# Optimization experiments

Measured on AMD Instinct MI355X. Metric: run time of the kernel, lower is better.

Reference implementation:

```python
import jax, jax.numpy as jnp
import numpy as np

DIM = 768
HEADS = 12
HEAD_DIM = DIM // HEADS
HIDDEN = 4 * DIM
SCALE = HEAD_DIM ** -0.5
LN_EPS = 1e-5


def layer_norm(x, g, b):
    mu = jnp.mean(x, axis=-1, keepdims=True)
    var = jnp.var(x, axis=-1, keepdims=True)
    return (x - mu) * jax.lax.rsqrt(var + LN_EPS) * g + b


def setup_inputs() -> dict:
    key = jax.random.key(0)
    ks = jax.random.split(key, 10)
    B, N = 2, 2048
    s = 0.02
    return {
        "x": jax.random.normal(ks[0], (B, N, DIM), jnp.float32),
        "elevation": jax.random.uniform(ks[1], (B, N), jnp.float32),
        "qkv_w": jax.random.normal(ks[2], (DIM, 3 * DIM), jnp.float32) * s,
        "qkv_b": jnp.zeros((3 * DIM,), jnp.float32),
        "proj_w": jax.random.normal(ks[3], (DIM, DIM), jnp.float32) * s,
        "proj_b": jnp.zeros((DIM,), jnp.float32),
        "ln1_g": jnp.ones((DIM,), jnp.float32),
        "ln1_b": jnp.zeros((DIM,), jnp.float32),
        "ln2_g": jnp.ones((DIM,), jnp.float32),
        "ln2_b": jnp.zeros((DIM,), jnp.float32),
        "fc1_w": jax.random.normal(ks[4], (DIM, HIDDEN), jnp.float32) * s,
        "fc1_b": jnp.zeros((HIDDEN,), jnp.float32),
        "fc2_w": jax.random.normal(ks[5], (HIDDEN, DIM), jnp.float32) * s,
        "fc2_b": jnp.zeros((DIM,), jnp.float32),
        "barrier": jnp.asarray(3.0, jnp.float32),
    }


def reference(x, elevation, qkv_w, qkv_b, proj_w, proj_b, ln1_g, ln1_b,
              ln2_g, ln2_b, fc1_w, fc1_b, fc2_w, fc2_b, barrier):
    B, N, C = x.shape
    h = layer_norm(x, ln1_g, ln1_b)
    qkv = (h @ qkv_w + qkv_b).reshape(B, N, 3, HEADS, HEAD_DIM)
    q, k, v = jnp.moveaxis(qkv, 2, 0)  # each [B, N, H, D]
    # scores: [B, H, N, N]
    scores = jnp.einsum('bnhd,bmhd->bhnm', q, k) * SCALE
    w = jax.nn.softmax(scores, axis=-1)
    # pairwise elevation mask [B, N, N]: sigmoid(-s * (elev_j - elev_i))
    diff = elevation[:, None, :] - elevation[:, :, None]
    mask = jnp.clip(jax.nn.sigmoid(-barrier * diff), 1e-6, 1.0)
    w = w * mask[:, None, :, :]
    w = w / (jnp.sum(w, axis=-1, keepdims=True) + 1e-8)
    attn_out = jnp.einsum('bhnm,bmhd->bnhd', w, v).reshape(B, N, C)
    x = x + attn_out @ proj_w + proj_b
    h2 = layer_norm(x, ln2_g, ln2_b)
    mlp = jax.nn.gelu(h2 @ fc1_w + fc1_b, approximate=False) @ fc2_w + fc2_b
    return x + mlp
```

## Files before the change

kernel.cpp:

```cpp
#include <hip/hip_runtime.h>
#include <math.h>

#define DIM 768
#define HEADS 12
#define SEQ 2048
#define ROWS 4096
#define LN_EPS 1e-5f

typedef __attribute__((ext_vector_type(8))) short short8;
typedef __attribute__((ext_vector_type(4))) float floatx4;
typedef __attribute__((ext_vector_type(16))) float floatx16;
typedef unsigned short ushort_t;

__device__ __forceinline__ ushort_t f2bf(float x) {
    unsigned u = __float_as_uint(x);
    u += 0x7fff + ((u >> 16) & 1);
    return (ushort_t)(u >> 16);
}

__device__ __forceinline__ void gload_lds16(const void* g, void* l) {
    __builtin_amdgcn_global_load_lds((const __attribute__((address_space(1))) void*)g,
                                     (__attribute__((address_space(3))) void*)l, 16, 0, 0);
}

__launch_bounds__(256)
__global__ void prep_all(const float* __restrict__ w0, const float* __restrict__ w1,
                         const float* __restrict__ w2, const float* __restrict__ w3,
                         ushort_t* __restrict__ t0, ushort_t* __restrict__ t1,
                         ushort_t* __restrict__ t2, ushort_t* __restrict__ t3,
                         const float* __restrict__ elev, const float* __restrict__ barrier_p,
                         float* __restrict__ G, float* __restrict__ C2,
                         const float* __restrict__ x, const float* __restrict__ ln1_g,
                         const float* __restrict__ ln1_b, ushort_t* __restrict__ h) {
    __shared__ __align__(16) ushort_t s[64][72];
    int bid = blockIdx.x;
    int t = threadIdx.x;
    if (bid < 1728) {
        const float* W; ushort_t* WT; int K, N, nx, id;
        if (bid < 432)       { W = w0; WT = t0; K = 768;  N = 2304; nx = 36; id = bid; }
        else if (bid < 576)  { W = w1; WT = t1; K = 768;  N = 768;  nx = 12; id = bid - 432; }
        else if (bid < 1152) { W = w2; WT = t2; K = 768;  N = 3072; nx = 48; id = bid - 576; }
        else                 { W = w3; WT = t3; K = 3072; N = 768;  nx = 12; id = bid - 1152; }
        int tx = id % nx, ty = id / nx;
        int k0 = ty * 64, n0 = tx * 64;
        int rr0 = t >> 4, c4 = (t & 15) * 4;
        for (int rr = rr0; rr < 64; rr += 16) {
            float4 w = *(const float4*)(W + (size_t)(k0 + rr) * N + n0 + c4);
            s[c4 + 0][rr] = f2bf(w.x); s[c4 + 1][rr] = f2bf(w.y);
            s[c4 + 2][rr] = f2bf(w.z); s[c4 + 3][rr] = f2bf(w.w);
        }
        __syncthreads();
        int nl = t >> 2, kq = (t & 3) * 16;
        uint4 a = *(const uint4*)&s[nl][kq];
        uint4 b = *(const uint4*)&s[nl][kq + 8];
        *(uint4*)(WT + (size_t)(n0 + nl) * K + k0 + kq) = a;
        *(uint4*)(WT + (size_t)(n0 + nl) * K + k0 + kq + 8) = b;
    } else if (bid < 1744) {
        int i = (bid - 1728) * 256 + t;
        float be = barrier_p[0] * elev[i];
        G[i]  = __expf(be);
        C2[i] = be;
    } else {
        int row = bid - 1744;
        const float* xr = x + (size_t)row * DIM;
        float v0 = xr[t], v1 = xr[t + 256], v2 = xr[t + 512];
        float sm  = v0 + v1 + v2;
        float ss = v0 * v0 + v1 * v1 + v2 * v2;
        #pragma unroll
        for (int o = 32; o >= 1; o >>= 1) { sm += __shfl_xor(sm, o); ss += __shfl_xor(ss, o); }
        __shared__ float rs[4], rss[4];
        int wid = t >> 6, lane = t & 63;
        if (lane == 0) { rs[wid] = sm; rss[wid] = ss; }
        __syncthreads();
        if (t == 0) {
            float S = 0.f, SS = 0.f;
            for (int i2 = 0; i2 < 4; i2++) { S += rs[i2]; SS += rss[i2]; }
            rs[0] = S; rss[0] = SS;
        }
        __syncthreads();
        float mean = rs[0] * (1.0f / DIM);
        float var  = rss[0] * (1.0f / DIM) - mean * mean;
        float rstd = rsqrtf(var + LN_EPS);
        ushort_t* orow = h + (size_t)row * DIM;
        orow[t]       = f2bf((v0 - mean) * rstd * ln1_g[t]       + ln1_b[t]);
        orow[t + 256] = f2bf((v1 - mean) * rstd * ln1_g[t + 256] + ln1_b[t + 256]);
        orow[t + 512] = f2bf((v2 - mean) * rstd * ln1_g[t + 512] + ln1_b[t + 512]);
    }
}

__launch_bounds__(256)
__global__ void ln_kernel(const float* __restrict__ x, const float* __restrict__ g,
                          const float* __restrict__ b, ushort_t* __restrict__ out) {
    int row = blockIdx.x;
    const float* xr = x + (size_t)row * DIM;
    int t = threadIdx.x;
    float v0 = xr[t], v1 = xr[t + 256], v2 = xr[t + 512];
    float s  = v0 + v1 + v2;
    float ss = v0 * v0 + v1 * v1 + v2 * v2;
    #pragma unroll
    for (int o = 32; o >= 1; o >>= 1) { s += __shfl_xor(s, o); ss += __shfl_xor(ss, o); }
    __shared__ float rs[4], rss[4];
    int wid = t >> 6, lane = t & 63;
    if (lane == 0) { rs[wid] = s; rss[wid] = ss; }
    __syncthreads();
    if (t == 0) {
        float S = 0.f, SS = 0.f;
        for (int i = 0; i < 4; i++) { S += rs[i]; SS += rss[i]; }
        rs[0] = S; rss[0] = SS;
    }
    __syncthreads();
    float mean = rs[0] * (1.0f / DIM);
    float var  = rss[0] * (1.0f / DIM) - mean * mean;
    float rstd = rsqrtf(var + LN_EPS);
    ushort_t* orow = out + (size_t)row * DIM;
    orow[t]       = f2bf((v0 - mean) * rstd * g[t]       + b[t]);
    orow[t + 256] = f2bf((v1 - mean) * rstd * g[t + 256] + b[t + 256]);
    orow[t + 512] = f2bf((v2 - mean) * rstd * g[t + 512] + b[t + 512]);
}


#define G16_PREFETCH(K0, SA, SB)                                                      \
    {                                                                                 \
        int c0_ = t, r0_ = c0_ >> 2, bl0_ = c0_ & 3;                                  \
        int sw0_ = bl0_ ^ ((r0_ ^ (r0_ >> 2)) & 3);                                   \
        gload_lds16(A  + (size_t)(row0 + r0_) * K + (K0) + (sw0_ << 3), &SA[c0_ * 8]); \
        gload_lds16(WT + (size_t)(col0 + r0_) * K + (K0) + (sw0_ << 3), &SB[c0_ * 8]); \
        int c1_ = 256 + t, r1_ = c1_ >> 2, bl1_ = c1_ & 3;                            \
        int sw1_ = bl1_ ^ ((r1_ ^ (r1_ >> 2)) & 3);                                   \
        gload_lds16(A  + (size_t)(row0 + r1_) * K + (K0) + (sw1_ << 3), &SA[c1_ * 8]); \
        gload_lds16(WT + (size_t)(col0 + r1_) * K + (K0) + (sw1_ << 3), &SB[c1_ * 8]); \
    }

#define G16_COMPUTE(SA, SB)                                                           \
    {                                                                                 \
        short8 a_[4], b_[4];                                                          \
        _Pragma("unroll")                                                             \
        for (int i = 0; i < 4; i++) {                                                 \
            int ra_ = wm * 64 + i * 16 + cl;                                          \
            a_[i] = *(const short8*)&SA[ra_ * 32 + ((quad ^ ((ra_ ^ (ra_ >> 2)) & 3)) << 3)]; \
        }                                                                             \
        _Pragma("unroll")                                                             \
        for (int j = 0; j < 4; j++) {                                                 \
            int rb_ = wn * 64 + j * 16 + cl;                                          \
            b_[j] = *(const short8*)&SB[rb_ * 32 + ((quad ^ ((rb_ ^ (rb_ >> 2)) & 3)) << 3)]; \
        }                                                                             \
        _Pragma("unroll")                                                             \
        for (int i = 0; i < 4; i++)                                                   \
            _Pragma("unroll")                                                         \
            for (int j = 0; j < 4; j++)                                               \
                acc[i][j] = __builtin_amdgcn_mfma_f32_16x16x32_bf16(a_[i], b_[j], acc[i][j], 0, 0, 0); \
    }

template<int EPI>
__launch_bounds__(256)
__global__ void gemm16(const ushort_t* __restrict__ A, const ushort_t* __restrict__ WT,
                       const float* __restrict__ bias, ushort_t* __restrict__ outB,
                       ushort_t* __restrict__ qb, ushort_t* __restrict__ kb,
                       ushort_t* __restrict__ vb, int N, int K) {
    __shared__ __align__(16) ushort_t sA0[128 * 32];
    __shared__ __align__(16) ushort_t sA1[128 * 32];
    __shared__ __align__(16) ushort_t sB0[128 * 32];
    __shared__ __align__(16) ushort_t sB1[128 * 32];
    int t = threadIdx.x;
    int row0 = blockIdx.y * 128, col0 = blockIdx.x * 128;
    int wid = t >> 6, lane = t & 63;
    int wm = wid >> 1, wn = wid & 1;
    int cl = lane & 15, quad = lane >> 4;

    floatx4 acc[4][4];
    #pragma unroll
    for (int i = 0; i < 4; i++)
        #pragma unroll
        for (int j = 0; j < 4; j++) { floatx4 z = {0.f, 0.f, 0.f, 0.f}; acc[i][j] = z; }

    G16_PREFETCH(0, sA0, sB0)
    for (int k0 = 0; k0 < K; k0 += 64) {
        __syncthreads();
        if (k0 + 32 < K) G16_PREFETCH(k0 + 32, sA1, sB1)
        G16_COMPUTE(sA0, sB0)
        __syncthreads();
        if (k0 + 64 < K) G16_PREFETCH(k0 + 64, sA0, sB0)
        G16_COMPUTE(sA1, sB1)
    }

    #pragma unroll
    for (int i = 0; i < 4; i++) {
        #pragma unroll
        for (int j = 0; j < 4; j++) {
            int gcol = col0 + wn * 64 + j * 16 + cl;
            float bv = bias[gcol];
            #pragma unroll
            for (int rg = 0; rg < 4; rg++) {
                int grow = row0 + wm * 64 + i * 16 + quad * 4 + rg;
                float v = acc[i][j][rg] + bv;
                if (EPI == 0) {
                    int which = gcol / 768;
                    int hc = gcol - which * 768;
                    int hh = hc >> 6, d = hc & 63;
                    int b_ = grow >> 11, n = grow & 2047;
                    size_t bhh = (size_t)(b_ * 12 + hh);
                    if (which == 0)      qb[(bhh * 2048 + n) * 64 + d] = f2bf(v * 0.125f);
                    else if (which == 1) kb[(bhh * 2048 + n) * 64 + d] = f2bf(v);
                    else                 vb[(bhh * 64 + d) * 2048 + n] = f2bf(v);
                } else {
                    v = 0.5f * v * (1.f + erff(v * 0.70710678118654752f));
                    outB[(size_t)grow * N + gcol] = f2bf(v);
                }
            }
        }
    }
}

#define GB_PREFETCH(K0, SA, SB)                                                       \
    {                                                                                 \
        int r_ = t >> 2, sub_ = t & 3;                                                \
        gload_lds16(A  + (size_t)(row0 + r_) * K + (K0) + sub_ * 8, &SA[t * 8]);      \
        gload_lds16(WT + (size_t)(col0 + r_) * K + (K0) + sub_ * 8, &SB[t * 8]);      \
    }

#define GB_COMPUTE(SA, SB)                                                            \
    {                                                                                 \
        short8 a_[2], b_[2];                                                          \
        _Pragma("unroll")                                                             \
        for (int i = 0; i < 2; i++)                                                   \
            a_[i] = *(const short8*)&SA[(wm * 32 + i * 16 + cl) * 32 + quad * 8];     \
        _Pragma("unroll")                                                             \
        for (int j = 0; j < 2; j++)                                                   \
            b_[j] = *(const short8*)&SB[(wn * 32 + j * 16 + cl) * 32 + quad * 8];     \
        _Pragma("unroll")                                                             \
        for (int i = 0; i < 2; i++)                                                   \
            _Pragma("unroll")                                                         \
            for (int j = 0; j < 2; j++)                                               \
                acc[i][j] = __builtin_amdgcn_mfma_f32_16x16x32_bf16(a_[i], b_[j], acc[i][j], 0, 0, 0); \
    }

__launch_bounds__(256)
__global__ void gemm_bf16(const ushort_t* __restrict__ A, const ushort_t* __restrict__ WT,
                          const float* __restrict__ bias, const float* __restrict__ res,
                          float* __restrict__ outF, int N, int K) {
    __shared__ __align__(16) ushort_t sA0[64 * 32];
    __shared__ __align__(16) ushort_t sA1[64 * 32];
    __shared__ __align__(16) ushort_t sB0[64 * 32];
    __shared__ __align__(16) ushort_t sB1[64 * 32];
    int t = threadIdx.x;
    int row0 = blockIdx.y * 64, col0 = blockIdx.x * 64;
    int wid = t >> 6, lane = t & 63;
    int wm = wid >> 1, wn = wid & 1;
    int cl = lane & 15, quad = lane >> 4;

    floatx4 acc[2][2];
    #pragma unroll
    for (int i = 0; i < 2; i++)
        #pragma unroll
        for (int j = 0; j < 2; j++) { floatx4 z = {0.f, 0.f, 0.f, 0.f}; acc[i][j] = z; }

    GB_PREFETCH(0, sA0, sB0)
    for (int k0 = 0; k0 < K; k0 += 64) {
        __syncthreads();
        if (k0 + 32 < K) GB_PREFETCH(k0 + 32, sA1, sB1)
        GB_COMPUTE(sA0, sB0)
        __syncthreads();
        if (k0 + 64 < K) GB_PREFETCH(k0 + 64, sA0, sB0)
        GB_COMPUTE(sA1, sB1)
    }

    #pragma unroll
    for (int i = 0; i < 2; i++) {
        #pragma unroll
        for (int j = 0; j < 2; j++) {
            int gcol = col0 + wn * 32 + j * 16 + cl;
            float bv = bias[gcol];
            #pragma unroll
            for (int rg = 0; rg < 4; rg++) {
                int grow = row0 + wm * 32 + i * 16 + quad * 4 + rg;
                float v = acc[i][j][rg] + bv + res[(size_t)grow * N + gcol];
                outF[(size_t)grow * N + gcol] = v;
            }
        }
    }
}

#define PREFETCH(K0N, KSN, VTN)                                                   \
    {                                                                             \
        const ushort_t* kbase_ = kb + (bh * 2048 + (K0N)) * 64;                   \
        const ushort_t* vbase_ = vb + bh * 131072 + (K0N);                        \
        int c0_ = t, r0_ = c0_ >> 3, b0_ = c0_ & 7;                               \
        gload_lds16(kbase_ + (r0_ << 6) + ((b0_ ^ (r0_ & 7)) << 3), &KSN[c0_ * 8]); \
        gload_lds16(vbase_ + (size_t)r0_ * 2048 + ((b0_ ^ (r0_ & 7)) << 3), &VTN[c0_ * 8]); \
        int c1_ = 256 + t, r1_ = c1_ >> 3, b1_ = c1_ & 7;                         \
        gload_lds16(kbase_ + (r1_ << 6) + ((b1_ ^ (r1_ & 7)) << 3), &KSN[c1_ * 8]); \
        gload_lds16(vbase_ + (size_t)r1_ * 2048 + ((b1_ ^ (r1_ & 7)) << 3), &VTN[c1_ * 8]); \
    }

#define ATTN_TILE(KT, KSC, VTC, KSN, VTN)                                         \
    {                                                                             \
        __syncthreads();                                                          \
        if ((KT) < 31) PREFETCH(((KT) + 1) * 64, KSN, VTN)                        \
        float gjv_[4];                                                            \
        gjv_[0] = G[b * 2048 + (KT) * 64 + cl];                                   \
        gjv_[1] = G[b * 2048 + (KT) * 64 + 16 + cl];                              \
        gjv_[2] = G[b * 2048 + (KT) * 64 + 32 + cl];                              \
        gjv_[3] = G[b * 2048 + (KT) * 64 + 48 + cl];                              \
        floatx4 s_[4];                                                            \
        s_[0] = c2init; s_[1] = c2init; s_[2] = c2init; s_[3] = c2init;           \
        _Pragma("unroll")                                                         \
        for (int kh = 0; kh < 2; kh++) {                                          \
            short8 aq_ = *(const short8*)&Qs[((wid * 16 + cl) << 6) + (((kh * 4 + quad) ^ (cl & 7)) << 3)]; \
            _Pragma("unroll")                                                     \
            for (int nt = 0; nt < 4; nt++) {                                      \
                short8 bk_ = *(const short8*)&KSC[((nt * 16 + cl) << 6) + (((kh * 4 + quad) ^ (cl & 7)) << 3)]; \
                s_[nt] = __builtin_amdgcn_mfma_f32_16x16x32_bf16(aq_, bk_, s_[nt], 0, 0, 0); \
            }                                                                     \
        }                                                                         \
        _Pragma("unroll")                                                         \
        for (int rg = 0; rg < 4; rg++) {                                          \
            int prow_ = wid * 16 + quad * 4 + rg;                                 \
            int r8_ = prow_ & 7, pb_ = prow_ << 6, cs_ = cl & 7, ch_ = cl >> 3;   \
            _Pragma("unroll")                                                     \
            for (int nt = 0; nt < 4; nt++) {                                      \
                float tf_ = __expf(s_[nt][rg]);                                   \
                float p_  = tf_ * __builtin_amdgcn_rcpf(gi[rg] + gjv_[nt]);       \
                sem[rg] += p_;                                                    \
                Ps[pb_ + (((nt * 2 + ch_) ^ r8_) << 3) + cs_] = (ushort_t)(__float_as_uint(p_) >> 16); \
            }                                                                     \
        }                                                                         \
        _Pragma("unroll")                                                         \
        for (int kh = 0; kh < 2; kh++) {                                          \
            short8 ap_ = *(const short8*)&Ps[((wid * 16 + cl) << 6) + (((kh * 4 + quad) ^ (cl & 7)) << 3)]; \
            _Pragma("unroll")                                                     \
            for (int dt = 0; dt < 4; dt++) {                                      \
                short8 bv_ = *(const short8*)&VTC[((dt * 16 + cl) << 6) + (((kh * 4 + quad) ^ (cl & 7)) << 3)]; \
                o[dt] = __builtin_amdgcn_mfma_f32_16x16x32_bf16(ap_, bv_, o[dt], 0, 0, 0); \
            }                                                                     \
        }                                                                         \
    }

__launch_bounds__(256)
__global__ void attn_mfma(const ushort_t* __restrict__ qb, const ushort_t* __restrict__ kb,
                          const ushort_t* __restrict__ vb, const float* __restrict__ G,
                          const float* __restrict__ C2, ushort_t* __restrict__ attn) {
    __shared__ __align__(16) ushort_t Qs[4096];
    __shared__ __align__(16) ushort_t Ks0[4096];
    __shared__ __align__(16) ushort_t Ks1[4096];
    __shared__ __align__(16) ushort_t Vt0[4096];
    __shared__ __align__(16) ushort_t Vt1[4096];
    __shared__ __align__(16) ushort_t Ps[4096];
    int qt = blockIdx.x, h = blockIdx.y, b = blockIdx.z;
    int t = threadIdx.x, wid = t >> 6, lane = t & 63;
    int cl = lane & 15, quad = lane >> 4;
    int q0 = qt * 64;
    size_t bh = (size_t)(b * 12 + h);

    const ushort_t* qbase = qb + (bh * 2048 + q0) * 64;
    #pragma unroll
    for (int i = 0; i < 2; i++) {
        int c = i * 256 + t, row = c >> 3, blk = c & 7;
        gload_lds16(qbase + (row << 6) + ((blk ^ (row & 7)) << 3), &Qs[c * 8]);
    }
    int qrow4 = b * 2048 + q0 + wid * 16 + quad * 4;
    float4 g4  = *(const float4*)(G  + qrow4);
    float4 c24 = *(const float4*)(C2 + qrow4);
    float gi[4]  = {g4.x, g4.y, g4.z, g4.w};
    floatx4 c2init = {c24.x, c24.y, c24.z, c24.w};

    PREFETCH(0, Ks0, Vt0)

    floatx4 o[4];
    #pragma unroll
    for (int j = 0; j < 4; j++) { floatx4 z = {0.f, 0.f, 0.f, 0.f}; o[j] = z; }
    float sem[4] = {0.f, 0.f, 0.f, 0.f};

    for (int kt = 0; kt < 32; kt += 2) {
        ATTN_TILE(kt,     Ks0, Vt0, Ks1, Vt1)
        ATTN_TILE(kt + 1, Ks1, Vt1, Ks0, Vt0)
    }

    #pragma unroll
    for (int rg = 0; rg < 4; rg++) {
        float m = sem[rg];
        #pragma unroll
        for (int off = 1; off < 16; off <<= 1) m += __shfl_xor(m, off);
        float inv = __builtin_amdgcn_rcpf(m);
        int grow = b * 2048 + q0 + wid * 16 + quad * 4 + rg;
        #pragma unroll
        for (int dt = 0; dt < 4; dt++)
            attn[(size_t)grow * 768 + h * 64 + dt * 16 + cl] = f2bf(o[dt][rg] * inv);
    }
}

extern "C" void kernel_launch(void* const* d_in, const int* in_sizes, int n_in,
                              void* d_out, int out_size, void* d_ws, size_t ws_size,
                              hipStream_t stream) {
    const float* x      = (const float*)d_in[0];
    const float* elev   = (const float*)d_in[1];
    const float* qkv_w  = (const float*)d_in[2];
    const float* qkv_b  = (const float*)d_in[3];
    const float* proj_w = (const float*)d_in[4];
    const float* proj_b = (const float*)d_in[5];
    const float* ln1_g  = (const float*)d_in[6];
    const float* ln1_b  = (const float*)d_in[7];
    const float* ln2_g  = (const float*)d_in[8];
    const float* ln2_b  = (const float*)d_in[9];
    const float* fc1_w  = (const float*)d_in[10];
    const float* fc1_b  = (const float*)d_in[11];
    const float* fc2_w  = (const float*)d_in[12];
    const float* fc2_b  = (const float*)d_in[13];
    const float* barrier= (const float*)d_in[14];
    float* out = (float*)d_out;
    char* ws = (char*)d_ws;

    ushort_t* h    = (ushort_t*)(ws + 0);
    ushort_t* qb   = (ushort_t*)(ws + 6291456);
    ushort_t* kb   = (ushort_t*)(ws + 12582912);
    ushort_t* vb   = (ushort_t*)(ws + 18874368);
    ushort_t* f1   = (ushort_t*)(ws + 0);
    ushort_t* attn = (ushort_t*)(ws + 25165824);
    ushort_t* h2   = (ushort_t*)(ws + 31457280);
    float*    Gf   = (float*)(ws + 31457280);
    float*    C2f  = (float*)(ws + 31473664);
    ushort_t* qkvT = (ushort_t*)(ws + 37748736);
    ushort_t* projT= (ushort_t*)(ws + 41287680);
    ushort_t* fc1T = (ushort_t*)(ws + 42467328);
    ushort_t* fc2T = (ushort_t*)(ws + 47185920);

    prep_all<<<5840, 256, 0, stream>>>(qkv_w, proj_w, fc1_w, fc2_w, qkvT, projT, fc1T, fc2T,
                                       elev, barrier, Gf, C2f, x, ln1_g, ln1_b, h);
    gemm16<0><<<dim3(2304 / 128, 32), 256, 0, stream>>>(
        h, qkvT, qkv_b, nullptr, qb, kb, vb, 2304, 768);
    attn_mfma<<<dim3(32, HEADS, 2), 256, 0, stream>>>(qb, kb, vb, Gf, C2f, attn);
    gemm_bf16<<<dim3(768 / 64, 64), 256, 0, stream>>>(
        attn, projT, proj_b, x, out, 768, 768);
    ln_kernel<<<ROWS, 256, 0, stream>>>(out, ln2_g, ln2_b, h2);
    gemm16<1><<<dim3(3072 / 128, 32), 256, 0, stream>>>(
        h2, fc1T, fc1_b, f1, nullptr, nullptr, nullptr, 3072, 768);
    gemm_bf16<<<dim3(768 / 64, 64), 256, 0, stream>>>(
        f1, fc2T, fc2_b, out, out, 768, 3072);
}
```

Measured before the change: 312.8 us.

## Load GEMM A fragments from global into registers, hoist attention Q fragments

In both GEMM kernels the A operand no longer goes through LDS. Each wave loads its A fragments straight from global memory into registers, one K-step ahead, while B stays double-buffered in LDS. This halves LDS traffic and LDS footprint, but the two waves that share the same A rows now each fetch them from global/L2, and the accesses are strided 16-byte row reads. In the attention kernel, the Q fragments are read from LDS once into registers before the loop, and the per-tile barrier moves from the start of each tile to its end.

```diff
diff --git a/kernel.cpp b/kernel.cpp
--- a/kernel.cpp
+++ b/kernel.cpp
@@ -9,7 +9,6 @@
 
 typedef __attribute__((ext_vector_type(8))) short short8;
 typedef __attribute__((ext_vector_type(4))) float floatx4;
-typedef __attribute__((ext_vector_type(16))) float floatx16;
 typedef unsigned short ushort_t;
 
 __device__ __forceinline__ ushort_t f2bf(float x) {
@@ -119,36 +118,35 @@
 }
 
 
-#define G16_PREFETCH(K0, SA, SB)                                                      \
+#define G16_PREB(K0, SB)                                                              \
     {                                                                                 \
         int c0_ = t, r0_ = c0_ >> 2, bl0_ = c0_ & 3;                                  \
         int sw0_ = bl0_ ^ ((r0_ ^ (r0_ >> 2)) & 3);                                   \
-        gload_lds16(A  + (size_t)(row0 + r0_) * K + (K0) + (sw0_ << 3), &SA[c0_ * 8]); \
         gload_lds16(WT + (size_t)(col0 + r0_) * K + (K0) + (sw0_ << 3), &SB[c0_ * 8]); \
         int c1_ = 256 + t, r1_ = c1_ >> 2, bl1_ = c1_ & 3;                            \
         int sw1_ = bl1_ ^ ((r1_ ^ (r1_ >> 2)) & 3);                                   \
-        gload_lds16(A  + (size_t)(row0 + r1_) * K + (K0) + (sw1_ << 3), &SA[c1_ * 8]); \
         gload_lds16(WT + (size_t)(col0 + r1_) * K + (K0) + (sw1_ << 3), &SB[c1_ * 8]); \
     }
 
-#define G16_COMPUTE(SA, SB)                                                           \
-    {                                                                                 \
-        short8 a_[4], b_[4];                                                          \
-        _Pragma("unroll")                                                             \
-        for (int i = 0; i < 4; i++) {                                                 \
-            int ra_ = wm * 64 + i * 16 + cl;                                          \
-            a_[i] = *(const short8*)&SA[ra_ * 32 + ((quad ^ ((ra_ ^ (ra_ >> 2)) & 3)) << 3)]; \
+#define G16_LOADA(K0, AR)                                                             \
+    {                                                                                 \
+        _Pragma("unroll")                                                             \
+        for (int i_ = 0; i_ < 4; i_++) AR[i_] = *(const short8*)(Arow[i_] + (K0));    \
+    }
+
+#define G16_COMP(AR, SB)                                                              \
+    {                                                                                 \
+        short8 b_[4];                                                                 \
+        _Pragma("unroll")                                                             \
+        for (int j_ = 0; j_ < 4; j_++) {                                              \
+            int rb_ = wn * 64 + j_ * 16 + cl;                                         \
+            b_[j_] = *(const short8*)&SB[rb_ * 32 + ((quad ^ ((rb_ ^ (rb_ >> 2)) & 3)) << 3)]; \
         }                                                                             \
         _Pragma("unroll")                                                             \
-        for (int j = 0; j < 4; j++) {                                                 \
-            int rb_ = wn * 64 + j * 16 + cl;                                          \
-            b_[j] = *(const short8*)&SB[rb_ * 32 + ((quad ^ ((rb_ ^ (rb_ >> 2)) & 3)) << 3)]; \
-        }                                                                             \
-        _Pragma("unroll")                                                             \
-        for (int i = 0; i < 4; i++)                                                   \
+        for (int i_ = 0; i_ < 4; i_++)                                                \
             _Pragma("unroll")                                                         \
-            for (int j = 0; j < 4; j++)                                               \
-                acc[i][j] = __builtin_amdgcn_mfma_f32_16x16x32_bf16(a_[i], b_[j], acc[i][j], 0, 0, 0); \
+            for (int j_ = 0; j_ < 4; j_++)                                            \
+                acc[i_][j_] = __builtin_amdgcn_mfma_f32_16x16x32_bf16(AR[i_], b_[j_], acc[i_][j_], 0, 0, 0); \
     }
 
 template<int EPI>
@@ -157,8 +155,6 @@
                        const float* __restrict__ bias, ushort_t* __restrict__ outB,
                        ushort_t* __restrict__ qb, ushort_t* __restrict__ kb,
                        ushort_t* __restrict__ vb, int N, int K) {
-    __shared__ __align__(16) ushort_t sA0[128 * 32];
-    __shared__ __align__(16) ushort_t sA1[128 * 32];
     __shared__ __align__(16) ushort_t sB0[128 * 32];
     __shared__ __align__(16) ushort_t sB1[128 * 32];
     int t = threadIdx.x;
@@ -167,20 +163,29 @@
     int wm = wid >> 1, wn = wid & 1;
     int cl = lane & 15, quad = lane >> 4;
 
+    const ushort_t* Arow[4];
+    #pragma unroll
+    for (int i = 0; i < 4; i++)
+        Arow[i] = A + (size_t)(row0 + wm * 64 + i * 16 + cl) * K + quad * 8;
+
     floatx4 acc[4][4];
     #pragma unroll
     for (int i = 0; i < 4; i++)
         #pragma unroll
         for (int j = 0; j < 4; j++) { floatx4 z = {0.f, 0.f, 0.f, 0.f}; acc[i][j] = z; }
 
-    G16_PREFETCH(0, sA0, sB0)
+    short8 aA[4], aB[4];
+    G16_PREB(0, sB0)
+    G16_LOADA(0, aA)
     for (int k0 = 0; k0 < K; k0 += 64) {
         __syncthreads();
-        if (k0 + 32 < K) G16_PREFETCH(k0 + 32, sA1, sB1)
-        G16_COMPUTE(sA0, sB0)
-        __syncthreads();
-        if (k0 + 64 < K) G16_PREFETCH(k0 + 64, sA0, sB0)
-        G16_COMPUTE(sA1, sB1)
+        if (k0 + 32 < K) G16_PREB(k0 + 32, sB1)
+        G16_LOADA(k0 + 32 < K ? k0 + 32 : 0, aB)
+        G16_COMP(aA, sB0)
+        __syncthreads();
+        if (k0 + 64 < K) G16_PREB(k0 + 64, sB0)
+        G16_LOADA(k0 + 64 < K ? k0 + 64 : 0, aA)
+        G16_COMP(aB, sB1)
     }
 
     #pragma unroll
@@ -211,35 +216,35 @@
     }
 }
 
-#define GB_PREFETCH(K0, SA, SB)                                                       \
+#define GB_PREB(K0, SB)                                                               \
     {                                                                                 \
         int r_ = t >> 2, sub_ = t & 3;                                                \
-        gload_lds16(A  + (size_t)(row0 + r_) * K + (K0) + sub_ * 8, &SA[t * 8]);      \
         gload_lds16(WT + (size_t)(col0 + r_) * K + (K0) + sub_ * 8, &SB[t * 8]);      \
     }
 
-#define GB_COMPUTE(SA, SB)                                                            \
-    {                                                                                 \
-        short8 a_[2], b_[2];                                                          \
-        _Pragma("unroll")                                                             \
-        for (int i = 0; i < 2; i++)                                                   \
-            a_[i] = *(const short8*)&SA[(wm * 32 + i * 16 + cl) * 32 + quad * 8];     \
-        _Pragma("unroll")                                                             \
-        for (int j = 0; j < 2; j++)                                                   \
-            b_[j] = *(const short8*)&SB[(wn * 32 + j * 16 + cl) * 32 + quad * 8];     \
-        _Pragma("unroll")                                                             \
-        for (int i = 0; i < 2; i++)                                                   \
+#define GB_LOADA(K0, AR)                                                              \
+    {                                                                                 \
+        _Pragma("unroll")                                                             \
+        for (int i_ = 0; i_ < 2; i_++) AR[i_] = *(const short8*)(Arow[i_] + (K0));    \
+    }
+
+#define GB_COMP(AR, SB)                                                               \
+    {                                                                                 \
+        short8 b_[2];                                                                 \
+        _Pragma("unroll")                                                             \
+        for (int j_ = 0; j_ < 2; j_++)                                                \
+            b_[j_] = *(const short8*)&SB[(wn * 32 + j_ * 16 + cl) * 32 + quad * 8];   \
+        _Pragma("unroll")                                                             \
+        for (int i_ = 0; i_ < 2; i_++)                                                \
             _Pragma("unroll")                                                         \
-            for (int j = 0; j < 2; j++)                                               \
-                acc[i][j] = __builtin_amdgcn_mfma_f32_16x16x32_bf16(a_[i], b_[j], acc[i][j], 0, 0, 0); \
+            for (int j_ = 0; j_ < 2; j_++)                                            \
+                acc[i_][j_] = __builtin_amdgcn_mfma_f32_16x16x32_bf16(AR[i_], b_[j_], acc[i_][j_], 0, 0, 0); \
     }
 
 __launch_bounds__(256)
 __global__ void gemm_bf16(const ushort_t* __restrict__ A, const ushort_t* __restrict__ WT,
                           const float* __restrict__ bias, const float* __restrict__ res,
                           float* __restrict__ outF, int N, int K) {
-    __shared__ __align__(16) ushort_t sA0[64 * 32];
-    __shared__ __align__(16) ushort_t sA1[64 * 32];
     __shared__ __align__(16) ushort_t sB0[64 * 32];
     __shared__ __align__(16) ushort_t sB1[64 * 32];
     int t = threadIdx.x;
@@ -248,20 +253,29 @@
     int wm = wid >> 1, wn = wid & 1;
     int cl = lane & 15, quad = lane >> 4;
 
+    const ushort_t* Arow[2];
+    #pragma unroll
+    for (int i = 0; i < 2; i++)
+        Arow[i] = A + (size_t)(row0 + wm * 32 + i * 16 + cl) * K + quad * 8;
+
     floatx4 acc[2][2];
     #pragma unroll
     for (int i = 0; i < 2; i++)
         #pragma unroll
         for (int j = 0; j < 2; j++) { floatx4 z = {0.f, 0.f, 0.f, 0.f}; acc[i][j] = z; }
 
-    GB_PREFETCH(0, sA0, sB0)
+    short8 aA[2], aB[2];
+    GB_PREB(0, sB0)
+    GB_LOADA(0, aA)
     for (int k0 = 0; k0 < K; k0 += 64) {
         __syncthreads();
-        if (k0 + 32 < K) GB_PREFETCH(k0 + 32, sA1, sB1)
-        GB_COMPUTE(sA0, sB0)
-        __syncthreads();
-        if (k0 + 64 < K) GB_PREFETCH(k0 + 64, sA0, sB0)
-        GB_COMPUTE(sA1, sB1)
+        if (k0 + 32 < K) GB_PREB(k0 + 32, sB1)
+        GB_LOADA(k0 + 32 < K ? k0 + 32 : 0, aB)
+        GB_COMP(aA, sB0)
+        __syncthreads();
+        if (k0 + 64 < K) GB_PREB(k0 + 64, sB0)
+        GB_LOADA(k0 + 64 < K ? k0 + 64 : 0, aA)
+        GB_COMP(aB, sB1)
     }
 
     #pragma unroll
@@ -294,7 +308,6 @@
 
 #define ATTN_TILE(KT, KSC, VTC, KSN, VTN)                                         \
     {                                                                             \
-        __syncthreads();                                                          \
         if ((KT) < 31) PREFETCH(((KT) + 1) * 64, KSN, VTN)                        \
         float gjv_[4];                                                            \
         gjv_[0] = G[b * 2048 + (KT) * 64 + cl];                                   \
@@ -305,7 +318,7 @@
         s_[0] = c2init; s_[1] = c2init; s_[2] = c2init; s_[3] = c2init;           \
         _Pragma("unroll")                                                         \
         for (int kh = 0; kh < 2; kh++) {                                          \
-            short8 aq_ = *(const short8*)&Qs[((wid * 16 + cl) << 6) + (((kh * 4 + quad) ^ (cl & 7)) << 3)]; \
+            short8 aq_ = (kh == 0) ? aq0 : aq1;                                   \
             _Pragma("unroll")                                                     \
             for (int nt = 0; nt < 4; nt++) {                                      \
                 short8 bk_ = *(const short8*)&KSC[((nt * 16 + cl) << 6) + (((kh * 4 + quad) ^ (cl & 7)) << 3)]; \
@@ -333,6 +346,7 @@
                 o[dt] = __builtin_amdgcn_mfma_f32_16x16x32_bf16(ap_, bv_, o[dt], 0, 0, 0); \
             }                                                                     \
         }                                                                         \
+        __syncthreads();                                                          \
     }
 
 __launch_bounds__(256)
@@ -364,6 +378,10 @@
     floatx4 c2init = {c24.x, c24.y, c24.z, c24.w};
 
     PREFETCH(0, Ks0, Vt0)
+    __syncthreads();
+
+    short8 aq0 = *(const short8*)&Qs[((wid * 16 + cl) << 6) + ((quad ^ (cl & 7)) << 3)];
+    short8 aq1 = *(const short8*)&Qs[((wid * 16 + cl) << 6) + (((4 + quad) ^ (cl & 7)) << 3)];
 
     floatx4 o[4];
     #pragma unroll
```

After: 400.4 us. 1.28x slower.

## Use 128x128 GEMM tiles for residual GEMMs and hoist Q fragments in attention

Applied to the files above, without the earlier changes.

Replaces the 64x64-tile gemm_bf16 kernel for the proj and fc2 GEMMs with a new residual-add epilogue mode of the 128x128-tile gemm16 kernel. This gives more reuse per LDS load but only 192 blocks for the N=768 outputs, which may underfill the GPU. In attention, the Q fragments are loaded into registers once before the loop instead of being re-read from LDS every tile. The barrier moves to the end of each tile, with an explicit sync after the initial prefetch.

```diff
diff --git a/kernel.cpp b/kernel.cpp
--- a/kernel.cpp
+++ b/kernel.cpp
@@ -9,7 +9,6 @@
 
 typedef __attribute__((ext_vector_type(8))) short short8;
 typedef __attribute__((ext_vector_type(4))) float floatx4;
-typedef __attribute__((ext_vector_type(16))) float floatx16;
 typedef unsigned short ushort_t;
 
 __device__ __forceinline__ ushort_t f2bf(float x) {
@@ -155,6 +154,7 @@
 __launch_bounds__(256)
 __global__ void gemm16(const ushort_t* __restrict__ A, const ushort_t* __restrict__ WT,
                        const float* __restrict__ bias, ushort_t* __restrict__ outB,
+                       const float* __restrict__ res, float* __restrict__ outF,
                        ushort_t* __restrict__ qb, ushort_t* __restrict__ kb,
                        ushort_t* __restrict__ vb, int N, int K) {
     __shared__ __align__(16) ushort_t sA0[128 * 32];
@@ -202,79 +202,13 @@
                     if (which == 0)      qb[(bhh * 2048 + n) * 64 + d] = f2bf(v * 0.125f);
                     else if (which == 1) kb[(bhh * 2048 + n) * 64 + d] = f2bf(v);
                     else                 vb[(bhh * 64 + d) * 2048 + n] = f2bf(v);
-                } else {
+                } else if (EPI == 1) {
                     v = 0.5f * v * (1.f + erff(v * 0.70710678118654752f));
                     outB[(size_t)grow * N + gcol] = f2bf(v);
+                } else {
+                    v += res[(size_t)grow * N + gcol];
+                    outF[(size_t)grow * N + gcol] = v;
                 }
-            }
-        }
-    }
-}
-
-#define GB_PREFETCH(K0, SA, SB)                                                       \
-    {                                                                                 \
-        int r_ = t >> 2, sub_ = t & 3;                                                \
-        gload_lds16(A  + (size_t)(row0 + r_) * K + (K0) + sub_ * 8, &SA[t * 8]);      \
-        gload_lds16(WT + (size_t)(col0 + r_) * K + (K0) + sub_ * 8, &SB[t * 8]);      \
-    }
-
-#define GB_COMPUTE(SA, SB)                                                            \
-    {                                                                                 \
-        short8 a_[2], b_[2];                                                          \
-        _Pragma("unroll")                                                             \
-        for (int i = 0; i < 2; i++)                                                   \
-            a_[i] = *(const short8*)&SA[(wm * 32 + i * 16 + cl) * 32 + quad * 8];     \
-        _Pragma("unroll")                                                             \
-        for (int j = 0; j < 2; j++)                                                   \
-            b_[j] = *(const short8*)&SB[(wn * 32 + j * 16 + cl) * 32 + quad * 8];     \
-        _Pragma("unroll")                                                             \
-        for (int i = 0; i < 2; i++)                                                   \
-            _Pragma("unroll")                                                         \
-            for (int j = 0; j < 2; j++)                                               \
-                acc[i][j] = __builtin_amdgcn_mfma_f32_16x16x32_bf16(a_[i], b_[j], acc[i][j], 0, 0, 0); \
-    }
-
-__launch_bounds__(256)
-__global__ void gemm_bf16(const ushort_t* __restrict__ A, const ushort_t* __restrict__ WT,
-                          const float* __restrict__ bias, const float* __restrict__ res,
-                          float* __restrict__ outF, int N, int K) {
-    __shared__ __align__(16) ushort_t sA0[64 * 32];
-    __shared__ __align__(16) ushort_t sA1[64 * 32];
-    __shared__ __align__(16) ushort_t sB0[64 * 32];
-    __shared__ __align__(16) ushort_t sB1[64 * 32];
-    int t = threadIdx.x;
-    int row0 = blockIdx.y * 64, col0 = blockIdx.x * 64;
-    int wid = t >> 6, lane = t & 63;
-    int wm = wid >> 1, wn = wid & 1;
-    int cl = lane & 15, quad = lane >> 4;
-
-    floatx4 acc[2][2];
-    #pragma unroll
-    for (int i = 0; i < 2; i++)
-        #pragma unroll
-        for (int j = 0; j < 2; j++) { floatx4 z = {0.f, 0.f, 0.f, 0.f}; acc[i][j] = z; }
-
-    GB_PREFETCH(0, sA0, sB0)
-    for (int k0 = 0; k0 < K; k0 += 64) {
-        __syncthreads();
-        if (k0 + 32 < K) GB_PREFETCH(k0 + 32, sA1, sB1)
-        GB_COMPUTE(sA0, sB0)
-        __syncthreads();
-        if (k0 + 64 < K) GB_PREFETCH(k0 + 64, sA0, sB0)
-        GB_COMPUTE(sA1, sB1)
-    }
-
-    #pragma unroll
-    for (int i = 0; i < 2; i++) {
-        #pragma unroll
-        for (int j = 0; j < 2; j++) {
-            int gcol = col0 + wn * 32 + j * 16 + cl;
-            float bv = bias[gcol];
-            #pragma unroll
-            for (int rg = 0; rg < 4; rg++) {
-                int grow = row0 + wm * 32 + i * 16 + quad * 4 + rg;
-                float v = acc[i][j][rg] + bv + res[(size_t)grow * N + gcol];
-                outF[(size_t)grow * N + gcol] = v;
             }
         }
     }
@@ -294,7 +228,6 @@
 
 #define ATTN_TILE(KT, KSC, VTC, KSN, VTN)                                         \
     {                                                                             \
-        __syncthreads();                                                          \
         if ((KT) < 31) PREFETCH(((KT) + 1) * 64, KSN, VTN)                        \
         float gjv_[4];                                                            \
         gjv_[0] = G[b * 2048 + (KT) * 64 + cl];                                   \
@@ -305,7 +238,7 @@
         s_[0] = c2init; s_[1] = c2init; s_[2] = c2init; s_[3] = c2init;           \
         _Pragma("unroll")                                                         \
         for (int kh = 0; kh < 2; kh++) {                                          \
-            short8 aq_ = *(const short8*)&Qs[((wid * 16 + cl) << 6) + (((kh * 4 + quad) ^ (cl & 7)) << 3)]; \
+            short8 aq_ = (kh == 0) ? aq0 : aq1;                                   \
             _Pragma("unroll")                                                     \
             for (int nt = 0; nt < 4; nt++) {                                      \
                 short8 bk_ = *(const short8*)&KSC[((nt * 16 + cl) << 6) + (((kh * 4 + quad) ^ (cl & 7)) << 3)]; \
@@ -333,6 +266,7 @@
                 o[dt] = __builtin_amdgcn_mfma_f32_16x16x32_bf16(ap_, bv_, o[dt], 0, 0, 0); \
             }                                                                     \
         }                                                                         \
+        __syncthreads();                                                          \
     }
 
 __launch_bounds__(256)
@@ -364,6 +298,10 @@
     floatx4 c2init = {c24.x, c24.y, c24.z, c24.w};
 
     PREFETCH(0, Ks0, Vt0)
+    __syncthreads();
+
+    short8 aq0 = *(const short8*)&Qs[((wid * 16 + cl) << 6) + ((quad ^ (cl & 7)) << 3)];
+    short8 aq1 = *(const short8*)&Qs[((wid * 16 + cl) << 6) + (((4 + quad) ^ (cl & 7)) << 3)];
 
     floatx4 o[4];
     #pragma unroll
@@ -425,14 +363,14 @@
 
     prep_all<<<5840, 256, 0, stream>>>(qkv_w, proj_w, fc1_w, fc2_w, qkvT, projT, fc1T, fc2T,
                                        elev, barrier, Gf, C2f, x, ln1_g, ln1_b, h);
-    gemm16<0><<<dim3(2304 / 128, 32), 256, 0, stream>>>(
-        h, qkvT, qkv_b, nullptr, qb, kb, vb, 2304, 768);
+    gemm16<0><<<dim3(18, 32), 256, 0, stream>>>(
+        h, qkvT, qkv_b, nullptr, nullptr, nullptr, qb, kb, vb, 2304, 768);
     attn_mfma<<<dim3(32, HEADS, 2), 256, 0, stream>>>(qb, kb, vb, Gf, C2f, attn);
-    gemm_bf16<<<dim3(768 / 64, 64), 256, 0, stream>>>(
-        attn, projT, proj_b, x, out, 768, 768);
+    gemm16<2><<<dim3(6, 32), 256, 0, stream>>>(
+        attn, projT, proj_b, nullptr, x, out, nullptr, nullptr, nullptr, 768, 768);
     ln_kernel<<<ROWS, 256, 0, stream>>>(out, ln2_g, ln2_b, h2);
-    gemm16<1><<<dim3(3072 / 128, 32), 256, 0, stream>>>(
-        h2, fc1T, fc1_b, f1, nullptr, nullptr, nullptr, 3072, 768);
-    gemm_bf16<<<dim3(768 / 64, 64), 256, 0, stream>>>(
-        f1, fc2T, fc2_b, out, out, 768, 3072);
-}
+    gemm16<1><<<dim3(24, 32), 256, 0, stream>>>(
+        h2, fc1T, fc1_b, f1, nullptr, nullptr, nullptr, nullptr, nullptr, 3072, 768);
+    gemm16<2><<<dim3(6, 32), 256, 0, stream>>>(
+        f1, fc2T, fc2_b, nullptr, out, out, nullptr, nullptr, nullptr, 768, 3072);
+}
```

Result: no change. 314.8 us (+0.6%).
